# Performance work log

Hardware: AMD Instinct MI355X
Metric: run time of the kernel (lower is better)

Reference implementation:

```python
import jax, jax.numpy as jnp
import numpy as np

D_MODEL = 1024
N_HEADS = 16
WINDOW = 64              # window_size
HEAD_DIM = D_MODEL // N_HEADS
HALF = WINDOW // 2
NWIN = WINDOW + 1        # half tokens each side + self
LN_EPS = 1e-5


def _layernorm(x, g, b):
    mu = jnp.mean(x, axis=-1, keepdims=True)
    var = jnp.var(x, axis=-1, keepdims=True)
    return (x - mu) * jax.lax.rsqrt(var + LN_EPS) * g + b


def _linear_attention(q, k, v):
    # feature map phi(x) = elu(x) + 1; O(n) attention over full d_model
    q = jax.nn.elu(q) + 1.0
    k = jax.nn.elu(k) + 1.0
    kv = jnp.einsum('bsd,bse->bde', k, v)          # [B, D, D]
    num = jnp.einsum('bsd,bde->bse', q, kv)        # [B, S, D]
    denom = jnp.einsum('bsd,bd->bs', q, k.sum(axis=1))
    return num / (denom[..., None] + 1e-6)


def _window_attention(q, k, v, rel_bias):
    # sliding window attention with relative position bias, banded via offset scan
    B, S, _ = q.shape
    qh = q.reshape(B, S, N_HEADS, HEAD_DIM).transpose(0, 2, 1, 3)  # [B,H,S,Dh]
    kh = k.reshape(B, S, N_HEADS, HEAD_DIM).transpose(0, 2, 1, 3)
    vh = v.reshape(B, S, N_HEADS, HEAD_DIM).transpose(0, 2, 1, 3)
    kp = jnp.pad(kh, ((0, 0), (0, 0), (HALF, HALF), (0, 0)))
    vp = jnp.pad(vh, ((0, 0), (0, 0), (HALF, HALF), (0, 0)))
    pos = jnp.arange(S)
    scale = np.float32(1.0 / np.sqrt(HEAD_DIM))

    def score_step(_, w):
        off = w - HALF                                   # relative offset in [-HALF, HALF]
        ks = jax.lax.dynamic_slice_in_dim(kp, w, S, axis=2)   # k at position i+off
        s = jnp.einsum('bhsd,bhsd->bhs', qh, ks) * scale
        s = s + rel_bias[off + WINDOW][None, :, None]    # bias per head for this offset
        valid = (pos + off >= 0) & (pos + off < S)
        s = jnp.where(valid[None, None, :], s, -jnp.inf)
        return None, s

    _, scores = jax.lax.scan(score_step, None, jnp.arange(NWIN))  # [W,B,H,S]
    attn = jax.nn.softmax(scores, axis=0)                          # softmax over window

    def out_step(acc, aw):
        a, w = aw
        vs = jax.lax.dynamic_slice_in_dim(vp, w, S, axis=2)
        return acc + a[..., None] * vs, None

    out, _ = jax.lax.scan(out_step, jnp.zeros_like(qh), (attn, jnp.arange(NWIN)))
    return out.transpose(0, 2, 1, 3).reshape(B, S, D_MODEL)


def setup_inputs() -> dict:
    key = jax.random.key(0)
    ks = jax.random.split(key, 16)

    def lin(k, fan_in, shape):
        return (jax.random.normal(k, shape, jnp.float32) / np.sqrt(fan_in)).astype(jnp.float32)

    D = D_MODEL
    inp = {
        'x': jax.random.normal(ks[0], (2, 2048, D), jnp.float32),
        'wq_lin': lin(ks[1], D, (D, D)), 'bq_lin': jnp.zeros((D,), jnp.float32),
        'wk_lin': lin(ks[2], D, (D, D)), 'bk_lin': jnp.zeros((D,), jnp.float32),
        'wv_lin': lin(ks[3], D, (D, D)), 'bv_lin': jnp.zeros((D,), jnp.float32),
        'wq_loc': lin(ks[4], D, (D, D)), 'bq_loc': jnp.zeros((D,), jnp.float32),
        'wk_loc': lin(ks[5], D, (D, D)), 'bk_loc': jnp.zeros((D,), jnp.float32),
        'wv_loc': lin(ks[6], D, (D, D)), 'bv_loc': jnp.zeros((D,), jnp.float32),
        'wo': lin(ks[7], D, (D, D)), 'bo': jnp.zeros((D,), jnp.float32),
        'wg1': lin(ks[8], 3 * D, (3 * D, D)), 'bg1': jnp.zeros((D,), jnp.float32),
        'wg2': lin(ks[9], D, (D, D)), 'bg2': jnp.zeros((D,), jnp.float32),
        'rel_bias': jax.random.normal(ks[10], (2 * WINDOW + 1, N_HEADS), jnp.float32),
        'ln_g': jnp.ones((D,), jnp.float32),
        'ln_b': jnp.zeros((D,), jnp.float32),
    }
    return inp


def reference(x, wq_lin, bq_lin, wk_lin, bk_lin, wv_lin, bv_lin,
              wq_loc, bq_loc, wk_loc, bk_loc, wv_loc, bv_loc,
              wo, bo, wg1, bg1, wg2, bg2, rel_bias, ln_g, ln_b):
    h = _layernorm(x, ln_g, ln_b)
    lin_out = _linear_attention(h @ wq_lin + bq_lin,
                                h @ wk_lin + bk_lin,
                                h @ wv_lin + bv_lin)
    win_out = _window_attention(h @ wq_loc + bq_loc,
                                h @ wk_loc + bk_loc,
                                h @ wv_loc + bv_loc, rel_bias)
    gate_in = jnp.concatenate([lin_out, win_out, h], axis=-1)
    gate = jax.nn.sigmoid(jnp.maximum(gate_in @ wg1 + bg1, 0.0) @ wg2 + bg2)
    out = gate * lin_out + (1.0 - gate) * win_out
    return out @ wo + bo + x
```

## Files before the change

### kernel.cpp

```cpp
#include <hip/hip_runtime.h>

typedef unsigned short u16;
typedef unsigned int u32;
typedef float f32x4 __attribute__((ext_vector_type(4)));
typedef __bf16 bf16x8 __attribute__((ext_vector_type(8)));

#define SEQ 2048
#define DM 1024

__device__ __forceinline__ float bf2f(u16 a){
  u32 b = ((u32)a) << 16; float f; __builtin_memcpy(&f, &b, 4); return f;
}
__device__ __forceinline__ u16 f2bf(float f){
  u32 b; __builtin_memcpy(&b, &f, 4);
  b += 0x7fffu + ((b >> 16) & 1u);
  return (u16)(b >> 16);
}

__device__ __forceinline__ void gload16(const void* g, void* l){
  __builtin_amdgcn_global_load_lds((const __attribute__((address_space(1))) u32*)g,
                                   (__attribute__((address_space(3))) u32*)l, 16, 0, 0);
}

#define SBAR  __builtin_amdgcn_sched_barrier(0); __builtin_amdgcn_s_barrier(); __builtin_amdgcn_sched_barrier(0);
#define VM0   asm volatile("s_waitcnt vmcnt(0)" ::: "memory"); __builtin_amdgcn_sched_barrier(0);
#define VM6   asm volatile("s_waitcnt vmcnt(6)" ::: "memory"); __builtin_amdgcn_sched_barrier(0);
#define VM8   asm volatile("s_waitcnt vmcnt(8)" ::: "memory"); __builtin_amdgcn_sched_barrier(0);

#define MFMA16(AF, BF) \
  __builtin_amdgcn_s_setprio(1); \
  _Pragma("unroll") for (int m_ = 0; m_ < 4; m_++) \
  _Pragma("unroll") for (int n_ = 0; n_ < 4; n_++) \
    acc[m_][n_] = __builtin_amdgcn_mfma_f32_16x16x32_bf16(AF[m_], BF[n_], acc[m_][n_], 0,0,0); \
  __builtin_amdgcn_s_setprio(0);

struct TP { const float* src[9]; u16* dst[9]; int K[9]; };

__global__ __launch_bounds__(256) void ktl(TP tp, const float* __restrict__ x,
                                           const float* __restrict__ gg, const float* __restrict__ bb,
                                           u16* __restrict__ h){
  __shared__ float tile[64][65];
  int z = blockIdx.z;
  int t = threadIdx.x;
  if (z == 9){
    int b0 = blockIdx.y * 16 + blockIdx.x;
    float* r1 = &tile[0][0];
    float* r2 = &tile[1][0];
    for (int row = b0; row < 4096; row += 768){
      float4 xv = ((const float4*)(x + (size_t)row * DM))[t];
      float s  = xv.x + xv.y + xv.z + xv.w;
      float s2 = xv.x*xv.x + xv.y*xv.y + xv.z*xv.z + xv.w*xv.w;
      #pragma unroll
      for (int o = 1; o < 64; o <<= 1){ s += __shfl_xor(s, o); s2 += __shfl_xor(s2, o); }
      if ((t & 63) == 0){ r1[t >> 6] = s; r2[t >> 6] = s2; }
      __syncthreads();
      float S = r1[0]+r1[1]+r1[2]+r1[3], S2 = r2[0]+r2[1]+r2[2]+r2[3];
      float mu = S * (1.0f/DM);
      float var = S2 * (1.0f/DM) - mu*mu;
      float rstd = rsqrtf(var + 1e-5f);
      float4 gv = ((const float4*)gg)[t], bv = ((const float4*)bb)[t];
      ushort4 o;
      o.x = f2bf((xv.x - mu)*rstd*gv.x + bv.x);
      o.y = f2bf((xv.y - mu)*rstd*gv.y + bv.y);
      o.z = f2bf((xv.z - mu)*rstd*gv.z + bv.z);
      o.w = f2bf((xv.w - mu)*rstd*gv.w + bv.w);
      ((ushort4*)(h + (size_t)row * DM))[t] = o;
      __syncthreads();
    }
    return;
  }
  int K = tp.K[z];
  int kb = blockIdx.y << 6, nb = blockIdx.x << 6;
  if (kb >= K) return;
  const float* W = tp.src[z];
  u16* WT = tp.dst[z];
  const int N = 1024;
  #pragma unroll
  for (int i = 0; i < 4; i++){
    int idx = t + (i << 8);
    int r = idx >> 4, c = (idx & 15) << 2;
    float4 v = *(const float4*)(W + (size_t)(kb + r) * N + nb + c);
    tile[r][c] = v.x; tile[r][c+1] = v.y; tile[r][c+2] = v.z; tile[r][c+3] = v.w;
  }
  __syncthreads();
  #pragma unroll
  for (int i = 0; i < 2; i++){
    int idx = t + (i << 8);
    int n = idx >> 3, k8 = (idx & 7) << 3;
    union { u16 s[8]; int4 v; } u;
    #pragma unroll
    for (int j = 0; j < 8; j++) u.s[j] = f2bf(tile[k8 + j][n]);
    *(int4*)(WT + (size_t)(nb + n) * K + kb + k8) = u.v;
  }
}

__device__ __forceinline__ float phi_elu(float v){ return v > 0.f ? v + 1.f : __expf(v); }

__global__ __launch_bounds__(512, 2) void kqkv8(
  const u16* __restrict__ h,
  const u16* wt0, const u16* wt1, const u16* wt2, const u16* wt3, const u16* wt4, const u16* wt5,
  const float* b0, const float* b1, const float* b2, const float* b3, const float* b4, const float* b5,
  u16* phiQ, u16* phiKT, u16* vT, u16* qloc, u16* kloc, u16* vlocT)
{
  extern __shared__ char smem[];
  char* LA0 = smem;
  char* LA1 = smem + 16384;
  char* LB0 = smem + 32768;
  char* LB1 = smem + 65536;

  const int t = threadIdx.x, lane = t & 63, w = t >> 6;
  const int wm = w >> 2, wn = w & 3;

  int bid = blockIdx.x;
  int swz = (bid & 7) * 96 + (bid >> 3);
  int mt = swz & 31, ntile = swz >> 5;
  int m0 = mt << 7;
  int n0g = ntile << 8;
  int wi = n0g >> 10;
  int n0 = n0g & 1023;
  const u16* Bp = wi==0?wt0: wi==1?wt1: wi==2?wt2: wi==3?wt3: wi==4?wt4: wt5;
  const float* bsel = wi==0?b0: wi==1?b1: wi==2?b2: wi==3?b3: wi==4?b4: b5;

  auto stageA = [&](char* dst, int kt){
    #pragma unroll
    for (int j = 0; j < 2; j++){
      int slot = (j << 9) + t;
      int r = slot >> 3;
      int csw = ((slot & 7) << 4) ^ ((r & 7) << 4);
      gload16((const char*)(h + (size_t)(m0 + r) * 1024 + (kt << 6)) + csw,
              dst + (((j << 9) + (w << 6)) << 4));
    }
  };
  auto stageB = [&](char* dst, int kt){
    #pragma unroll
    for (int j = 0; j < 4; j++){
      int slot = (j << 9) + t;
      int r = slot >> 3;
      int csw = ((slot & 7) << 4) ^ ((r & 7) << 4);
      gload16((const char*)(Bp + (size_t)(n0 + r) * 1024 + (kt << 6)) + csw,
              dst + (((j << 9) + (w << 6)) << 4));
    }
  };
  auto rdA = [&](const char* ab, int m, int kk) -> bf16x8 {
    int ra = (wm << 6) + (m << 4) + (lane & 15);
    return *(const bf16x8*)(ab + (ra << 7) + (((kk << 6) + ((lane >> 4) << 4)) ^ ((ra & 7) << 4)));
  };
  auto rdB = [&](const char* bb, int n, int kk) -> bf16x8 {
    int rb = (wn << 6) + (n << 4) + (lane & 15);
    return *(const bf16x8*)(bb + (rb << 7) + (((kk << 6) + ((lane >> 4) << 4)) ^ ((rb & 7) << 4)));
  };

  f32x4 acc[4][4];
  #pragma unroll
  for (int m = 0; m < 4; m++)
    #pragma unroll
    for (int n = 0; n < 4; n++) acc[m][n] = (f32x4){0.f,0.f,0.f,0.f};

  const int NT = 16;
  bf16x8 a0[4], bq0[4], a1[4], bq1[4];

  stageA(LA0, 0); stageB(LB0, 0);
  stageA(LA1, 1); stageB(LB1, 1);
  VM6 SBAR
  #pragma unroll
  for (int m = 0; m < 4; m++) a0[m] = rdA(LA0, m, 0);
  #pragma unroll
  for (int n = 0; n < 4; n++) bq0[n] = rdB(LB0, n, 0);

  #pragma unroll 1
  for (int i = 0; i < NT/2; i++){
    int e = 2*i, o = e + 1;
    int se = (e + 2 < NT) ? e + 2 : NT - 1;
    int so = (o + 2 < NT) ? o + 2 : NT - 1;
    #pragma unroll
    for (int m = 0; m < 4; m++) a1[m] = rdA(LA0, m, 1);
    #pragma unroll
    for (int n = 0; n < 4; n++) bq1[n] = rdB(LB0, n, 1);
    SBAR
    stageA(LA0, se); stageB(LB0, se);
    MFMA16(a0, bq0)
    VM6 SBAR
    #pragma unroll
    for (int m = 0; m < 4; m++) a0[m] = rdA(LA1, m, 0);
    #pragma unroll
    for (int n = 0; n < 4; n++) bq0[n] = rdB(LB1, n, 0);
    MFMA16(a1, bq1)
    #pragma unroll
    for (int m = 0; m < 4; m++) a1[m] = rdA(LA1, m, 1);
    #pragma unroll
    for (int n = 0; n < 4; n++) bq1[n] = rdB(LB1, n, 1);
    SBAR
    stageA(LA1, so); stageB(LB1, so);
    MFMA16(a0, bq0)
    VM6 SBAR
    if (i < NT/2 - 1){
      #pragma unroll
      for (int m = 0; m < 4; m++) a0[m] = rdA(LA0, m, 0);
      #pragma unroll
      for (int n = 0; n < 4; n++) bq0[n] = rdB(LB0, n, 0);
    }
    MFMA16(a1, bq1)
  }
  VM0

  #pragma unroll
  for (int n = 0; n < 4; n++){
    int col = n0 + (wn << 6) + (n << 4) + (lane & 15);
    float bv = bsel[col];
    #pragma unroll
    for (int m = 0; m < 4; m++){
      int r0 = m0 + (wm << 6) + (m << 4) + ((lane >> 4) << 2);
      float e[4];
      #pragma unroll
      for (int r = 0; r < 4; r++) e[r] = acc[m][n][r] + bv;
      if (wi == 0){
        #pragma unroll
        for (int r = 0; r < 4; r++) phiQ[(size_t)(r0 + r) * DM + col] = f2bf(phi_elu(e[r]));
      } else if (wi == 1 || wi == 2 || wi == 5){
        union { u16 s[4]; ushort4 v; } o;
        #pragma unroll
        for (int r = 0; r < 4; r++) o.s[r] = f2bf(wi == 1 ? phi_elu(e[r]) : e[r]);
        int bb = r0 >> 11, sl = r0 & 2047;
        u16* dst = (wi == 1) ? phiKT : (wi == 2 ? vT : vlocT);
        *(ushort4*)(dst + ((size_t)(bb << 10) + col) * SEQ + sl) = o.v;
      } else {
        u16* dst = wi==3 ? qloc : kloc;
        #pragma unroll
        for (int r = 0; r < 4; r++) dst[(size_t)(r0 + r) * DM + col] = f2bf(e[r]);
      }
    }
  }
}

template<int NCHUNK>
__device__ __forceinline__ void pipe128(const u16* A0c, const u16* A1c, const u16* A2c, int lda,
                                        const u16* B, int ldb, int K, int m0, int n0,
                                        char* LA0, char* LA1, char* LB0, char* LB1,
                                        f32x4 (&acc)[4][4])
{
  const int t = threadIdx.x, lane = t & 63, w = t >> 6;
  const int wm = w >> 1, wn = w & 1;
  const int NT = K >> 6;

  auto stageA = [&](char* dst, int kt){
    const u16* Ab;
    if (NCHUNK == 3){
      int ci = kt >> 4;
      const u16* cp = (ci == 0) ? A0c : ((ci == 1) ? A1c : A2c);
      Ab = cp + ((kt & 15) << 6);
    } else {
      Ab = A0c + (kt << 6);
    }
    #pragma unroll
    for (int j = 0; j < 4; j++){
      int slot = (j << 8) + t;
      int r = slot >> 3;
      int csw = ((slot & 7) << 4) ^ ((r & 7) << 4);
      gload16((const char*)(Ab + (size_t)(m0 + r) * lda) + csw,
              dst + (((j << 8) + (w << 6)) << 4));
    }
  };
  auto stageB = [&](char* dst, int kt){
    const u16* Bb = B + (kt << 6);
    #pragma unroll
    for (int j = 0; j < 4; j++){
      int slot = (j << 8) + t;
      int r = slot >> 3;
      int csw = ((slot & 7) << 4) ^ ((r & 7) << 4);
      gload16((const char*)(Bb + (size_t)(n0 + r) * ldb) + csw,
              dst + (((j << 8) + (w << 6)) << 4));
    }
  };
  auto rdA = [&](const char* ab, int m, int kk) -> bf16x8 {
    int ra = (wm << 6) + (m << 4) + (lane & 15);
    return *(const bf16x8*)(ab + (ra << 7) + (((kk << 6) + ((lane >> 4) << 4)) ^ ((ra & 7) << 4)));
  };
  auto rdB = [&](const char* bb, int n, int kk) -> bf16x8 {
    int rb = (wn << 6) + (n << 4) + (lane & 15);
    return *(const bf16x8*)(bb + (rb << 7) + (((kk << 6) + ((lane >> 4) << 4)) ^ ((rb & 7) << 4)));
  };

  bf16x8 a0[4], bq0[4], a1[4], bq1[4];

  stageA(LA0, 0); stageB(LB0, 0);
  stageA(LA1, 1); stageB(LB1, 1);
  VM8 SBAR
  #pragma unroll
  for (int m = 0; m < 4; m++) a0[m] = rdA(LA0, m, 0);
  #pragma unroll
  for (int n = 0; n < 4; n++) bq0[n] = rdB(LB0, n, 0);

  #pragma unroll 1
  for (int i = 0; i < NT/2; i++){
    int e = 2*i, o = e + 1;
    int se = (e + 2 < NT) ? e + 2 : NT - 1;
    int so = (o + 2 < NT) ? o + 2 : NT - 1;
    #pragma unroll
    for (int m = 0; m < 4; m++) a1[m] = rdA(LA0, m, 1);
    #pragma unroll
    for (int n = 0; n < 4; n++) bq1[n] = rdB(LB0, n, 1);
    SBAR
    stageA(LA0, se); stageB(LB0, se);
    MFMA16(a0, bq0)
    VM8 SBAR
    #pragma unroll
    for (int m = 0; m < 4; m++) a0[m] = rdA(LA1, m, 0);
    #pragma unroll
    for (int n = 0; n < 4; n++) bq0[n] = rdB(LB1, n, 0);
    MFMA16(a1, bq1)
    #pragma unroll
    for (int m = 0; m < 4; m++) a1[m] = rdA(LA1, m, 1);
    #pragma unroll
    for (int n = 0; n < 4; n++) bq1[n] = rdB(LB1, n, 1);
    SBAR
    stageA(LA1, so); stageB(LB1, so);
    MFMA16(a0, bq0)
    VM8 SBAR
    if (i < NT/2 - 1){
      #pragma unroll
      for (int m = 0; m < 4; m++) a0[m] = rdA(LA0, m, 0);
      #pragma unroll
      for (int n = 0; n < 4; n++) bq0[n] = rdB(LB0, n, 0);
    }
    MFMA16(a1, bq1)
  }
  VM0
}

#define PIPE_LDS \
  __shared__ char LA0[16384], LA1[16384], LB0[16384], LB1[16384];

#define EPI_COORDS \
  const int lane = threadIdx.x & 63, w = threadIdx.x >> 6; \
  const int wm = w >> 1, wn = w & 1;

#define ZERO_ACC f32x4 acc[4][4]; \
  _Pragma("unroll") for (int m = 0; m < 4; m++) _Pragma("unroll") for (int n = 0; n < 4; n++) acc[m][n] = (f32x4){0.f,0.f,0.f,0.f};

__global__ __launch_bounds__(256) void kkvw(
  const u16* __restrict__ vT, const u16* __restrict__ phiKT,
  u16* __restrict__ kvp0, u16* __restrict__ kvp1,
  const u16* __restrict__ qloc, const u16* __restrict__ kloc,
  const u16* __restrict__ vlocT, const float* __restrict__ rel_bias,
  u16* __restrict__ wout, float* __restrict__ ks)
{
  extern __shared__ char sm[];
  const int t = threadIdx.x, lane = t & 63, w = t >> 6;
  int bid = blockIdx.x;
  if (bid < 256){
    int mt = bid & 7, nt = (bid >> 3) & 7, b = (bid >> 6) & 1, kh = bid >> 7;
    int m0 = mt << 7, n0 = nt << 7;
    const u16* A = vT + (size_t)b * DM * SEQ + (kh << 10);
    const u16* B = phiKT + (size_t)b * DM * SEQ + (kh << 10);
    char* LA0 = sm; char* LA1 = sm + 16384; char* LB0 = sm + 32768; char* LB1 = sm + 49152;
    ZERO_ACC
    pipe128<1>(A, 0, 0, SEQ, B, SEQ, 1024, m0, n0, LA0, LA1, LB0, LB1, acc);
    const int wm = w >> 1, wn = w & 1;
    u16* C = (kh ? kvp1 : kvp0) + (size_t)b * DM * DM;
    #pragma unroll
    for (int n = 0; n < 4; n++){
      int col = n0 + wn*64 + n*16 + (lane & 15);
      #pragma unroll
      for (int m = 0; m < 4; m++){
        int r0 = m0 + wm*64 + m*16 + ((lane >> 4) << 2);
        #pragma unroll
        for (int r = 0; r < 4; r++) C[(size_t)(r0 + r) * DM + col] = f2bf(acc[m][n][r]);
      }
    }
    return;
  }
  if (bid >= 1280){
    int row = bid - 1280;
    float* red = (float*)sm;
    const ushort4* src = (const ushort4*)(phiKT + (size_t)row * SEQ);
    float s = 0.f;
    for (int i = t; i < 512; i += 256){
      ushort4 v = src[i];
      s += bf2f(v.x) + bf2f(v.y) + bf2f(v.z) + bf2f(v.w);
    }
    #pragma unroll
    for (int o = 1; o < 64; o <<= 1) s += __shfl_xor(s, o);
    if ((t & 63) == 0) red[t >> 6] = s;
    __syncthreads();
    if (t == 0) ks[row] = red[0] + red[1] + red[2] + red[3];
    return;
  }
  char* Qs = sm;
  char* Ks = sm + 8192;
  char* Vs = sm + 24576;
  char* Ps = sm + 40960;
  float* bias_s = (float*)(sm + 57344);
  int i = bid - 256;
  int qt = i & 31, hh = (i >> 5) & 15, b = i >> 9;
  int q0 = qt << 6;
  size_t rowbase = (size_t)b * SEQ;

  #pragma unroll
  for (int j = 0; j < 2; j++){
    int c = (j << 8) + t;
    int row = c >> 3;
    int csw = ((c & 7) << 4) ^ ((row & 7) << 4);
    gload16((const char*)(qloc + (rowbase + q0 + row) * DM + hh*64) + csw,
            Qs + (((j << 8) + (w << 6)) << 4));
  }
  #pragma unroll
  for (int j = 0; j < 4; j++){
    int c = (j << 8) + t;
    int row = c >> 3;
    int csw = ((c & 7) << 4) ^ ((row & 7) << 4);
    int p = q0 + row - 32;
    p = p < 0 ? 0 : (p > SEQ-1 ? SEQ-1 : p);
    gload16((const char*)(kloc + (rowbase + p) * DM + hh*64) + csw,
            Ks + (((j << 8) + (w << 6)) << 4));
  }
  #pragma unroll
  for (int j = 0; j < 4; j++){
    int c = (j << 8) + t;
    int row = c >> 4;
    int csw = ((c & 15) << 4) ^ ((row & 7) << 4);
    int k0 = q0 - 32 + (csw >> 1);
    k0 = k0 < 0 ? 0 : (k0 > SEQ-8 ? SEQ-8 : k0);
    gload16((const char*)(vlocT + ((size_t)(b << 10) + hh*64 + row) * SEQ + k0),
            Vs + (((j << 8) + (w << 6)) << 4));
  }
  if (t < 65) bias_s[t] = rel_bias[(t + 32) * 16 + hh];
  __syncthreads();

  auto rdQ = [&](int kk) -> bf16x8 {
    int ra = (w << 4) + (lane & 15);
    return *(const bf16x8*)(Qs + (ra << 7) + (((kk << 6) + ((lane >> 4) << 4)) ^ ((ra & 7) << 4)));
  };
  auto rdK = [&](int n, int kk) -> bf16x8 {
    int rb = (n << 4) + (lane & 15);
    return *(const bf16x8*)(Ks + (rb << 7) + (((kk << 6) + ((lane >> 4) << 4)) ^ ((rb & 7) << 4)));
  };
  f32x4 sa[8];
  #pragma unroll
  for (int n = 0; n < 8; n++) sa[n] = (f32x4){0.f,0.f,0.f,0.f};
  {
    bf16x8 qf0 = rdQ(0), qf1 = rdQ(1);
    #pragma unroll
    for (int n = 0; n < 8; n++){
      sa[n] = __builtin_amdgcn_mfma_f32_16x16x32_bf16(qf0, rdK(n, 0), sa[n], 0,0,0);
      sa[n] = __builtin_amdgcn_mfma_f32_16x16x32_bf16(qf1, rdK(n, 1), sa[n], 0,0,0);
    }
  }

  int qrel = (w << 4) + ((lane >> 4) << 2);
  float m_[4] = {-1e30f, -1e30f, -1e30f, -1e30f};
  #pragma unroll
  for (int n = 0; n < 8; n++){
    int ridx = (n << 4) + (lane & 15);
    int p = q0 + ridx - 32;
    #pragma unroll
    for (int j = 0; j < 4; j++){
      int d = ridx - (qrel + j);
      bool ok = ((unsigned)d <= 64u) && ((unsigned)p < (unsigned)SEQ);
      float bb = bias_s[(unsigned)d <= 64u ? d : 0];
      float v = ok ? sa[n][j] * 0.125f + bb : -1e30f;
      sa[n][j] = v;
      m_[j] = fmaxf(m_[j], v);
    }
  }
  #pragma unroll
  for (int o = 1; o < 16; o <<= 1){
    #pragma unroll
    for (int j = 0; j < 4; j++) m_[j] = fmaxf(m_[j], __shfl_xor(m_[j], o));
  }
  float l_[4] = {0.f, 0.f, 0.f, 0.f};
  #pragma unroll
  for (int n = 0; n < 8; n++){
    #pragma unroll
    for (int j = 0; j < 4; j++){
      float e = __expf(sa[n][j] - m_[j]);
      sa[n][j] = e;
      l_[j] += e;
    }
  }
  #pragma unroll
  for (int o = 1; o < 16; o <<= 1){
    #pragma unroll
    for (int j = 0; j < 4; j++) l_[j] += __shfl_xor(l_[j], o);
  }

  #pragma unroll
  for (int n = 0; n < 8; n++){
    int colb = ((n << 4) + (lane & 15)) << 1;
    #pragma unroll
    for (int j = 0; j < 4; j++){
      int row = qrel + j;
      *(u16*)(Ps + (row << 8) + (colb ^ ((row & 7) << 4))) = f2bf(sa[n][j]);
    }
  }
  __syncthreads();

  auto rdP = [&](int kk) -> bf16x8 {
    int ra = (w << 4) + (lane & 15);
    return *(const bf16x8*)(Ps + (ra << 8) + (((kk << 6) + ((lane >> 4) << 4)) ^ ((ra & 7) << 4)));
  };
  auto rdV = [&](int n, int kk) -> bf16x8 {
    int rb = (n << 4) + (lane & 15);
    return *(const bf16x8*)(Vs + (rb << 8) + (((kk << 6) + ((lane >> 4) << 4)) ^ ((rb & 7) << 4)));
  };
  f32x4 oa[4];
  #pragma unroll
  for (int n = 0; n < 4; n++) oa[n] = (f32x4){0.f,0.f,0.f,0.f};
  #pragma unroll
  for (int kk = 0; kk < 4; kk++){
    bf16x8 pf = rdP(kk);
    #pragma unroll
    for (int n = 0; n < 4; n++)
      oa[n] = __builtin_amdgcn_mfma_f32_16x16x32_bf16(pf, rdV(n, kk), oa[n], 0,0,0);
  }

  #pragma unroll
  for (int j = 0; j < 4; j++){
    float inv = 1.0f / l_[j];
    int q = q0 + qrel + j;
    u16* dst = wout + (rowbase + q) * DM + hh*64;
    #pragma unroll
    for (int n = 0; n < 4; n++)
      dst[(n << 4) + (lane & 15)] = f2bf(oa[n][j] * inv);
  }
}

__global__ __launch_bounds__(256) void kdva(const u16* __restrict__ kvp0, const u16* __restrict__ kvp1,
                                            u16* __restrict__ kvT,
                                            const u16* __restrict__ phiQ, const float* __restrict__ ks,
                                            float* __restrict__ dn){
  int bid = blockIdx.x, t = threadIdx.x;
  if (bid < 1024){
    size_t i = ((size_t)bid * 256 + t) * 8;
    int4 ra = *(const int4*)(kvp0 + i);
    int4 rb = *(const int4*)(kvp1 + i);
    const u16* pa = (const u16*)&ra; const u16* pb = (const u16*)&rb;
    union { u16 s[8]; int4 v; } o;
    #pragma unroll
    for (int j = 0; j < 8; j++) o.s[j] = f2bf(bf2f(pa[j]) + bf2f(pb[j]));
    *(int4*)(kvT + i) = o.v;
    return;
  }
  int row = bid - 1024;
  ushort4 v = ((const ushort4*)(phiQ + (size_t)row * DM))[t];
  float4 kk = ((const float4*)(ks + ((size_t)(row >> 11) << 10)))[t];
  float s = bf2f(v.x)*kk.x + bf2f(v.y)*kk.y + bf2f(v.z)*kk.z + bf2f(v.w)*kk.w;
  #pragma unroll
  for (int o = 1; o < 64; o <<= 1) s += __shfl_xor(s, o);
  __shared__ float red[4];
  if ((t & 63) == 0) red[t >> 6] = s;
  __syncthreads();
  if (t == 0) dn[row] = red[0] + red[1] + red[2] + red[3];
}

__global__ __launch_bounds__(256) void knum(const u16* __restrict__ phiQ, const u16* __restrict__ kvT,
                                            const float* __restrict__ dn, u16* __restrict__ lin){
  PIPE_LDS
  int b = blockIdx.z;
  int m0 = blockIdx.x << 7, n0 = blockIdx.y << 7;
  const u16* A = phiQ + (size_t)b * SEQ * DM;
  const u16* B = kvT + (size_t)b * DM * DM;
  ZERO_ACC
  pipe128<1>(A, 0, 0, DM, B, DM, DM, m0, n0, LA0, LA1, LB0, LB1, acc);
  EPI_COORDS
  #pragma unroll
  for (int n = 0; n < 4; n++){
    int col = n0 + wn*64 + n*16 + (lane & 15);
    #pragma unroll
    for (int m = 0; m < 4; m++){
      int r0 = m0 + wm*64 + m*16 + ((lane >> 4) << 2);
      #pragma unroll
      for (int r = 0; r < 4; r++){
        float d = dn[(b << 11) + r0 + r] + 1e-6f;
        lin[((size_t)(b << 11) + r0 + r) * DM + col] = f2bf(acc[m][n][r] / d);
      }
    }
  }
}

__global__ __launch_bounds__(256) void kgate1(const u16* __restrict__ lin, const u16* __restrict__ win,
                                              const u16* __restrict__ h, const u16* __restrict__ wg1T,
                                              const float* __restrict__ bg1, u16* __restrict__ g1){
  PIPE_LDS
  int m0 = blockIdx.x << 7, n0 = blockIdx.y << 7;
  ZERO_ACC
  pipe128<3>(lin, win, h, DM, wg1T, 3072, 3072, m0, n0, LA0, LA1, LB0, LB1, acc);
  EPI_COORDS
  #pragma unroll
  for (int n = 0; n < 4; n++){
    int col = n0 + wn*64 + n*16 + (lane & 15);
    float bv = bg1[col];
    #pragma unroll
    for (int m = 0; m < 4; m++){
      int r0 = m0 + wm*64 + m*16 + ((lane >> 4) << 2);
      #pragma unroll
      for (int r = 0; r < 4; r++){
        float v = acc[m][n][r] + bv;
        g1[(size_t)(r0 + r) * DM + col] = f2bf(v > 0.f ? v : 0.f);
      }
    }
  }
}

__global__ __launch_bounds__(256) void kgate2(const u16* __restrict__ g1, const u16* __restrict__ wg2T,
                                              const float* __restrict__ bg2, const u16* __restrict__ lin,
                                              const u16* __restrict__ win, u16* __restrict__ outc){
  PIPE_LDS
  int m0 = blockIdx.x << 7, n0 = blockIdx.y << 7;
  ZERO_ACC
  pipe128<1>(g1, 0, 0, DM, wg2T, DM, DM, m0, n0, LA0, LA1, LB0, LB1, acc);
  EPI_COORDS
  #pragma unroll
  for (int n = 0; n < 4; n++){
    int col = n0 + wn*64 + n*16 + (lane & 15);
    float bv = bg2[col];
    #pragma unroll
    for (int m = 0; m < 4; m++){
      int r0 = m0 + wm*64 + m*16 + ((lane >> 4) << 2);
      #pragma unroll
      for (int r = 0; r < 4; r++){
        size_t idx = (size_t)(r0 + r) * DM + col;
        float g = 1.0f / (1.0f + __expf(-(acc[m][n][r] + bv)));
        float lv = bf2f(lin[idx]), wv = bf2f(win[idx]);
        outc[idx] = f2bf(g * lv + (1.0f - g) * wv);
      }
    }
  }
}

__global__ __launch_bounds__(256) void kfinal(const u16* __restrict__ outc, const u16* __restrict__ woT,
                                              const float* __restrict__ bo, const float* __restrict__ x,
                                              float* __restrict__ out){
  PIPE_LDS
  int m0 = blockIdx.x << 7, n0 = blockIdx.y << 7;
  ZERO_ACC
  pipe128<1>(outc, 0, 0, DM, woT, DM, DM, m0, n0, LA0, LA1, LB0, LB1, acc);
  EPI_COORDS
  #pragma unroll
  for (int n = 0; n < 4; n++){
    int col = n0 + wn*64 + n*16 + (lane & 15);
    float bv = bo[col];
    #pragma unroll
    for (int m = 0; m < 4; m++){
      int r0 = m0 + wm*64 + m*16 + ((lane >> 4) << 2);
      #pragma unroll
      for (int r = 0; r < 4; r++){
        size_t idx = (size_t)(r0 + r) * DM + col;
        out[idx] = acc[m][n][r] + bv + x[idx];
      }
    }
  }
}

extern "C" void kernel_launch(void* const* d_in, const int* in_sizes, int n_in,
                              void* d_out, int out_size, void* d_ws, size_t ws_size,
                              hipStream_t stream)
{
  const float* x      = (const float*)d_in[0];
  const float* wq_lin = (const float*)d_in[1];  const float* bq_lin = (const float*)d_in[2];
  const float* wk_lin = (const float*)d_in[3];  const float* bk_lin = (const float*)d_in[4];
  const float* wv_lin = (const float*)d_in[5];  const float* bv_lin = (const float*)d_in[6];
  const float* wq_loc = (const float*)d_in[7];  const float* bq_loc = (const float*)d_in[8];
  const float* wk_loc = (const float*)d_in[9];  const float* bk_loc = (const float*)d_in[10];
  const float* wv_loc = (const float*)d_in[11]; const float* bv_loc = (const float*)d_in[12];
  const float* wo     = (const float*)d_in[13]; const float* bo     = (const float*)d_in[14];
  const float* wg1    = (const float*)d_in[15]; const float* bg1    = (const float*)d_in[16];
  const float* wg2    = (const float*)d_in[17]; const float* bg2    = (const float*)d_in[18];
  const float* rel_bias = (const float*)d_in[19];
  const float* ln_g   = (const float*)d_in[20]; const float* ln_b   = (const float*)d_in[21];

  char* ws = (char*)d_ws;
  size_t off = 0;
  auto alloc = [&](size_t bytes) -> void* {
    void* p = ws + off;
    off += (bytes + 255) & ~(size_t)255;
    return p;
  };
  const size_t MB2 = (size_t)1024 * 1024 * 2;
  const size_t ACT = (size_t)4096 * 1024 * 2;
  u16* wT[6]; for (int i = 0; i < 6; i++) wT[i] = (u16*)alloc(MB2);
  u16* woT   = (u16*)alloc(MB2);
  u16* wg1T  = (u16*)alloc((size_t)1024 * 3072 * 2);
  u16* wg2T  = (u16*)alloc(MB2);
  u16* hbf   = (u16*)alloc(ACT);
  u16* phiQ  = (u16*)alloc(ACT);
  u16* phiKT = (u16*)alloc(ACT);
  u16* vT    = (u16*)alloc(ACT);
  u16* qloc  = (u16*)alloc(ACT);
  u16* kloc  = (u16*)alloc(ACT);
  u16* vlocT = (u16*)alloc(ACT);
  u16* kvT   = (u16*)alloc(2 * MB2);
  u16* kvp0  = (u16*)alloc(2 * MB2);
  u16* kvp1  = (u16*)alloc(2 * MB2);
  float* ksum = (float*)alloc(2 * 1024 * 4);
  float* dnm  = (float*)alloc(4096 * 4);
  u16* lin   = (u16*)alloc(ACT);
  u16* win   = (u16*)alloc(ACT);
  u16* g1    = phiQ;
  u16* outc  = vT;

  hipFuncSetAttribute((const void*)kqkv8, hipFuncAttributeMaxDynamicSharedMemorySize, 98304);
  hipFuncSetAttribute((const void*)kkvw, hipFuncAttributeMaxDynamicSharedMemorySize, 65536);

  dim3 blk(256);
  TP tp;
  tp.src[0]=wq_lin; tp.src[1]=wk_lin; tp.src[2]=wv_lin; tp.src[3]=wq_loc; tp.src[4]=wk_loc;
  tp.src[5]=wv_loc; tp.src[6]=wo; tp.src[7]=wg1; tp.src[8]=wg2;
  tp.dst[0]=wT[0]; tp.dst[1]=wT[1]; tp.dst[2]=wT[2]; tp.dst[3]=wT[3]; tp.dst[4]=wT[4];
  tp.dst[5]=wT[5]; tp.dst[6]=woT; tp.dst[7]=wg1T; tp.dst[8]=wg2T;
  for (int i = 0; i < 9; i++) tp.K[i] = (i == 7) ? 3072 : 1024;

  ktl<<<dim3(16,48,10), blk, 0, stream>>>(tp, x, ln_g, ln_b, hbf);

  kqkv8<<<768, 512, 98304, stream>>>(hbf, wT[0], wT[1], wT[2], wT[3], wT[4], wT[5],
                                     bq_lin, bk_lin, bv_lin, bq_loc, bk_loc, bv_loc,
                                     phiQ, phiKT, vT, qloc, kloc, vlocT);

  kkvw<<<3328, blk, 65536, stream>>>(vT, phiKT, kvp0, kvp1, qloc, kloc, vlocT, rel_bias, win, ksum);

  kdva<<<5120, blk, 0, stream>>>(kvp0, kvp1, kvT, phiQ, ksum, dnm);

  knum<<<dim3(16,8,2), blk, 0, stream>>>(phiQ, kvT, dnm, lin);

  kgate1<<<dim3(32,8), blk, 0, stream>>>(lin, win, hbf, wg1T, bg1, g1);
  kgate2<<<dim3(32,8), blk, 0, stream>>>(g1, wg2T, bg2, lin, win, outc);
  kfinal<<<dim3(32,8), blk, 0, stream>>>(outc, woT, bo, x, (float*)d_out);
}
```

Measured before the change: 214.7 us.

## Move output and gate weight transposes into the kv/window attention kernel

After: 220.2 us. +2.5%, slower.

```diff
diff --git a/kernel.cpp b/kernel.cpp
--- a/kernel.cpp
+++ b/kernel.cpp
@@ -34,7 +34,29 @@
     acc[m_][n_] = __builtin_amdgcn_mfma_f32_16x16x32_bf16(AF[m_], BF[n_], acc[m_][n_], 0,0,0); \
   __builtin_amdgcn_s_setprio(0);
 
-struct TP { const float* src[9]; u16* dst[9]; int K[9]; };
+__device__ __forceinline__ void trans_tile(const float* W, u16* WT, int K, int kb, int nb,
+                                           float (*tile)[65], int t){
+  const int N = 1024;
+  #pragma unroll
+  for (int i = 0; i < 4; i++){
+    int idx = t + (i << 8);
+    int r = idx >> 4, c = (idx & 15) << 2;
+    float4 v = *(const float4*)(W + (size_t)(kb + r) * N + nb + c);
+    tile[r][c] = v.x; tile[r][c+1] = v.y; tile[r][c+2] = v.z; tile[r][c+3] = v.w;
+  }
+  __syncthreads();
+  #pragma unroll
+  for (int i = 0; i < 2; i++){
+    int idx = t + (i << 8);
+    int n = idx >> 3, k8 = (idx & 7) << 3;
+    union { u16 s[8]; int4 v; } u;
+    #pragma unroll
+    for (int j = 0; j < 8; j++) u.s[j] = f2bf(tile[k8 + j][n]);
+    *(int4*)(WT + (size_t)(nb + n) * K + kb + k8) = u.v;
+  }
+}
+
+struct TP { const float* src[6]; u16* dst[6]; };
 
 __global__ __launch_bounds__(256) void ktl(TP tp, const float* __restrict__ x,
                                            const float* __restrict__ gg, const float* __restrict__ bb,
@@ -42,11 +64,11 @@
   __shared__ float tile[64][65];
   int z = blockIdx.z;
   int t = threadIdx.x;
-  if (z == 9){
+  if (z == 6){
     int b0 = blockIdx.y * 16 + blockIdx.x;
     float* r1 = &tile[0][0];
     float* r2 = &tile[1][0];
-    for (int row = b0; row < 4096; row += 768){
+    for (int row = b0; row < 4096; row += 256){
       float4 xv = ((const float4*)(x + (size_t)row * DM))[t];
       float s  = xv.x + xv.y + xv.z + xv.w;
       float s2 = xv.x*xv.x + xv.y*xv.y + xv.z*xv.z + xv.w*xv.w;
@@ -69,29 +91,7 @@
     }
     return;
   }
-  int K = tp.K[z];
-  int kb = blockIdx.y << 6, nb = blockIdx.x << 6;
-  if (kb >= K) return;
-  const float* W = tp.src[z];
-  u16* WT = tp.dst[z];
-  const int N = 1024;
-  #pragma unroll
-  for (int i = 0; i < 4; i++){
-    int idx = t + (i << 8);
-    int r = idx >> 4, c = (idx & 15) << 2;
-    float4 v = *(const float4*)(W + (size_t)(kb + r) * N + nb + c);
-    tile[r][c] = v.x; tile[r][c+1] = v.y; tile[r][c+2] = v.z; tile[r][c+3] = v.w;
-  }
-  __syncthreads();
-  #pragma unroll
-  for (int i = 0; i < 2; i++){
-    int idx = t + (i << 8);
-    int n = idx >> 3, k8 = (idx & 7) << 3;
-    union { u16 s[8]; int4 v; } u;
-    #pragma unroll
-    for (int j = 0; j < 8; j++) u.s[j] = f2bf(tile[k8 + j][n]);
-    *(int4*)(WT + (size_t)(nb + n) * K + kb + k8) = u.v;
-  }
+  trans_tile(tp.src[z], tp.dst[z], 1024, blockIdx.y << 6, blockIdx.x << 6, tile, t);
 }
 
 __device__ __forceinline__ float phi_elu(float v){ return v > 0.f ? v + 1.f : __expf(v); }
@@ -342,7 +342,9 @@
   u16* __restrict__ kvp0, u16* __restrict__ kvp1,
   const u16* __restrict__ qloc, const u16* __restrict__ kloc,
   const u16* __restrict__ vlocT, const float* __restrict__ rel_bias,
-  u16* __restrict__ wout, float* __restrict__ ks)
+  u16* __restrict__ wout, float* __restrict__ ks,
+  const float* __restrict__ wo_s, const float* __restrict__ wg1_s, const float* __restrict__ wg2_s,
+  u16* __restrict__ woT, u16* __restrict__ wg1T, u16* __restrict__ wg2T)
 {
   extern __shared__ char sm[];
   const int t = threadIdx.x, lane = t & 63, w = t >> 6;
@@ -366,6 +368,20 @@
         #pragma unroll
         for (int r = 0; r < 4; r++) C[(size_t)(r0 + r) * DM + col] = f2bf(acc[m][n][r]);
       }
+    }
+    return;
+  }
+  if (bid >= 3328){
+    float (*tile)[65] = (float(*)[65])sm;
+    int tid = bid - 3328;
+    if (tid < 256){
+      trans_tile(wo_s, woT, 1024, (tid >> 4) << 6, (tid & 15) << 6, tile, t);
+    } else if (tid < 512){
+      int q = tid - 256;
+      trans_tile(wg2_s, wg2T, 1024, (q >> 4) << 6, (q & 15) << 6, tile, t);
+    } else {
+      int q = tid - 512;
+      trans_tile(wg1_s, wg1T, 3072, (q >> 4) << 6, (q & 15) << 6, tile, t);
     }
     return;
   }
@@ -703,19 +719,17 @@
 
   dim3 blk(256);
   TP tp;
-  tp.src[0]=wq_lin; tp.src[1]=wk_lin; tp.src[2]=wv_lin; tp.src[3]=wq_loc; tp.src[4]=wk_loc;
-  tp.src[5]=wv_loc; tp.src[6]=wo; tp.src[7]=wg1; tp.src[8]=wg2;
-  tp.dst[0]=wT[0]; tp.dst[1]=wT[1]; tp.dst[2]=wT[2]; tp.dst[3]=wT[3]; tp.dst[4]=wT[4];
-  tp.dst[5]=wT[5]; tp.dst[6]=woT; tp.dst[7]=wg1T; tp.dst[8]=wg2T;
-  for (int i = 0; i < 9; i++) tp.K[i] = (i == 7) ? 3072 : 1024;
-
-  ktl<<<dim3(16,48,10), blk, 0, stream>>>(tp, x, ln_g, ln_b, hbf);
+  tp.src[0]=wq_lin; tp.src[1]=wk_lin; tp.src[2]=wv_lin; tp.src[3]=wq_loc; tp.src[4]=wk_loc; tp.src[5]=wv_loc;
+  tp.dst[0]=wT[0]; tp.dst[1]=wT[1]; tp.dst[2]=wT[2]; tp.dst[3]=wT[3]; tp.dst[4]=wT[4]; tp.dst[5]=wT[5];
+
+  ktl<<<dim3(16,16,7), blk, 0, stream>>>(tp, x, ln_g, ln_b, hbf);
 
   kqkv8<<<768, 512, 98304, stream>>>(hbf, wT[0], wT[1], wT[2], wT[3], wT[4], wT[5],
                                      bq_lin, bk_lin, bv_lin, bq_loc, bk_loc, bv_loc,
                                      phiQ, phiKT, vT, qloc, kloc, vlocT);
 
-  kkvw<<<3328, blk, 65536, stream>>>(vT, phiKT, kvp0, kvp1, qloc, kloc, vlocT, rel_bias, win, ksum);
+  kkvw<<<4608, blk, 65536, stream>>>(vT, phiKT, kvp0, kvp1, qloc, kloc, vlocT, rel_bias, win, ksum,
+                                     wo, wg1, wg2, woT, wg1T, wg2T);
 
   kdva<<<5120, blk, 0, stream>>>(kvp0, kvp1, kvT, phiQ, ksum, dnm);
 
```
